# Performance work log

Measured on AMD Instinct MI355X. Metric: run time of the kernel, lower is better.

## Reference

```python
import jax, jax.numpy as jnp
import numpy as np

N_NODES = 50000
N_EDGES = 500000
D_MODEL = 128
NHEAD = 8
D_HEAD = 16
NUM_KEYS = 8
NUM_ETYPES = 4
NUM_STRINGS = 20000
NUM_BLOCKS = 2
N_TARGETS = 128


def setup_inputs() -> dict:
    key = jax.random.key(0)
    ks = jax.random.split(key, 16)
    s = 1.0 / np.sqrt(D_MODEL)
    return {
        "emb": jax.random.normal(ks[0], (NUM_STRINGS, D_MODEL), jnp.float32) * s,
        "query_w": jax.random.normal(ks[1], (NUM_BLOCKS, NUM_KEYS, NHEAD, D_HEAD, D_MODEL), jnp.float32) * s,
        "key_w": jax.random.normal(ks[2], (NUM_BLOCKS, NUM_ETYPES, NHEAD, D_HEAD, D_MODEL), jnp.float32) * s,
        "value_w": jax.random.normal(ks[3], (NUM_BLOCKS, NUM_ETYPES, NHEAD, D_HEAD, D_MODEL), jnp.float32) * s,
        "node_w": jax.random.normal(ks[4], (NUM_BLOCKS, NUM_KEYS, NHEAD, D_HEAD, D_MODEL), jnp.float32) * s,
        "target_w": jax.random.normal(ks[5], (NUM_BLOCKS, NUM_KEYS, NHEAD, D_HEAD), jnp.float32) * s,
        "ln_gamma": jnp.ones((NUM_BLOCKS, D_MODEL), jnp.float32),
        "ln_beta": jnp.zeros((NUM_BLOCKS, D_MODEL), jnp.float32),
        "value_ids": jax.random.randint(ks[6], (N_NODES,), 0, NUM_STRINGS),
        "key_ids": jax.random.randint(ks[7], (N_NODES,), 0, NUM_KEYS),
        "src": jax.random.randint(ks[8], (N_EDGES,), 0, N_NODES),
        "dst": jax.random.randint(ks[9], (N_EDGES,), 0, N_NODES),
        "etype": jax.random.randint(ks[10], (N_EDGES,), 0, NUM_ETYPES),
        "target_idx": jax.random.randint(ks[11], (N_TARGETS,), 0, N_NODES),
    }


def _layer_norm(x, g, b, eps=1e-5):
    mu = jnp.mean(x, -1, keepdims=True)
    var = jnp.var(x, -1, keepdims=True)
    return (x - mu) * jax.lax.rsqrt(var + eps) * g + b


def _per_type_proj(feat, w, type_ids):
    # feat: [N,D], w: [T,H,Dh,D] -> project for all types then select the
    # node's/edge-endpoint's own type (identical math to gathering w[type]).
    all_t = jnp.einsum("nd,thfd->nthf", feat, w)  # [N,T,H,Dh]
    return jnp.take_along_axis(all_t, type_ids[:, None, None, None], axis=1)[:, 0]


def _hetero_attn_conv(feat, qw, kw, vw, nw, lg, lb, key_ids, src, dst, etype):
    n = feat.shape[0]
    q = _per_type_proj(feat, qw, key_ids)                     # [N,H,Dh] per-key query
    k_all = jnp.einsum("nd,thfd->nthf", feat, kw)             # [N,T,H,Dh]
    v_all = jnp.einsum("nd,thfd->nthf", feat, vw)
    k_e = k_all[src, etype]                                   # [E,H,Dh] per-etype key
    v_e = v_all[src, etype]                                   # [E,H,Dh]
    scale = np.float32(1.0 / np.sqrt(D_HEAD))
    scores = jnp.sum(q[dst] * k_e, -1) * scale                # [E,H]
    # edge softmax over incoming edges of each dst node
    m = jax.ops.segment_max(scores, dst, num_segments=n)      # [N,H]
    e = jnp.exp(scores - m[dst])
    z = jax.ops.segment_sum(e, dst, num_segments=n)
    attn = e / (z[dst] + 1e-9)                                # [E,H]
    agg = jax.ops.segment_sum(attn[..., None] * v_e, dst, num_segments=n)
    agg = agg.reshape(n, D_MODEL)
    h = _per_type_proj(agg, nw, key_ids).reshape(n, D_MODEL)  # per-key node proj
    h = jax.nn.relu(h)                                        # node_activation='relu'
    return _layer_norm(h, lg, lb)                             # norm=True


def reference(emb, query_w, key_w, value_w, node_w, target_w, ln_gamma, ln_beta,
              value_ids, key_ids, src, dst, etype, target_idx):
    feat = emb[value_ids]  # ValueEmbedding lookup [N,D]
    target_keys = key_ids[target_idx]
    outs = []
    for i in range(NUM_BLOCKS):
        prev = feat
        feat = _hetero_attn_conv(feat, query_w[i], key_w[i], value_w[i], node_w[i],
                                 ln_gamma[i], ln_beta[i], key_ids, src, dst, etype)
        feat = feat + prev  # block_residual=True (conv_residual=False)
        tf = feat[target_idx].reshape(N_TARGETS, NHEAD, D_HEAD)
        tw = target_w[i][target_keys]  # [B,H,Dh]
        outs.append(jnp.sum(tf * tw, axis=(1, 2)))  # Target readout per block
    out = jnp.mean(jnp.stack(outs, -1), -1)  # mean over block outputs
    return out  # [N_TARGETS] (single target)
```

## Files before the change

kernel.cpp:

```cpp
#include <hip/hip_runtime.h>
#include <hip/hip_bf16.h>

#define N_NODES   50000
#define N_EDGES   500000
#define NHEAD     8
#define NUM_KEYS  8
#define NUM_ETYPES 4
#define NUM_BLOCKS 2
#define N_TARGETS 128
#define NPAD      51200
#define NTILES    400
#define NBLK      196
#define LDW       136
#define LDWF      132
#define QKVW      1152
#define SCAP      45

typedef unsigned short u16;
typedef unsigned int   u32;
typedef __attribute__((ext_vector_type(8))) short short8;
typedef __attribute__((ext_vector_type(4))) short short4v;
typedef __attribute__((ext_vector_type(4))) float floatx4;

__device__ __forceinline__ size_t pkaddr(int tile, int r, int c){
  return (size_t)tile * 16384 + ((c >> 3) << 10) + (r << 3) + (c & 7);
}

__device__ __forceinline__ float bflo(u32 u)  { return __uint_as_float(u << 16); }
__device__ __forceinline__ float bfhi(u32 u)  { return __uint_as_float(u & 0xffff0000u); }
__device__ __forceinline__ float bf2f(u16 u)  { return __uint_as_float(((u32)u) << 16); }
__device__ __forceinline__ u16   f2bf(float f){
  u32 u = __float_as_uint(f);
  u += 0x7fffu + ((u >> 16) & 1u);
  return (u16)(u >> 16);
}

__global__ void detect_dtype(const u16* raw, int* flag){
  __shared__ int cnt;
  if (threadIdx.x == 0) cnt = 0;
  __syncthreads();
  int sane = 0;
  #pragma unroll
  for (int k = 0; k < 4; k++){
    u16 u = raw[threadIdx.x * 4 + k];
    int e = (u >> 7) & 0xff;
    if (e >= 100 && e <= 145) sane++;
  }
  atomicAdd(&cnt, sane);
  __syncthreads();
  if (threadIdx.x == 0) *flag = (cnt >= 870) ? 1 : 0;
}

__global__ void cvt_f32(const void* src, float* dst, int n, const int* flag){
  int i = blockIdx.x * 256 + threadIdx.x;
  if (i >= n) return;
  dst[i] = (*flag) ? bf2f(((const u16*)src)[i]) : ((const float*)src)[i];
}
__global__ void cvt_packw(const void* src, size_t soff, u16* dst, int n, const int* flag){
  int i = blockIdx.x * 256 + threadIdx.x;
  if (i >= n) return;
  u16 v = (*flag) ? ((const u16*)src)[soff + i] : f2bf(((const float*)src)[soff + i]);
  int mat = i >> 14, rem = i & 16383;
  int row = rem >> 7, k = rem & 127;
  dst[pkaddr(mat, row, k)] = v;
}

__global__ void khist_blk(const int* __restrict__ key_ids, int* __restrict__ blkcnt){
  __shared__ int c[8];
  int t = threadIdx.x, b = blockIdx.x;
  if (t < 8) c[t] = 0;
  __syncthreads();
  int n = b * 256 + t;
  if (n < N_NODES) atomicAdd(&c[key_ids[n]], 1);
  __syncthreads();
  if (t < 8) blkcnt[t * NBLK + b] = c[t];
}
__global__ void kscan2(const int* __restrict__ blkcnt, int* __restrict__ base,
                       int* __restrict__ tile_key){
  __shared__ int po[8];
  __shared__ int tot[8];
  int t = threadIdx.x;
  if (t < 8){
    int s = 0;
    for (int b = 0; b < NBLK; b++) s += blkcnt[t * NBLK + b];
    tot[t] = s;
  }
  __syncthreads();
  if (t == 0){
    int off = 0;
    for (int k = 0; k < 8; k++){ po[k] = off; off += ((tot[k] + 127) >> 7) << 7; }
  }
  __syncthreads();
  if (t < 8){
    int run = po[t];
    for (int b = 0; b < NBLK; b++){ base[t * NBLK + b] = run; run += blkcnt[t * NBLK + b]; }
  }
  for (int tt = t; tt < NTILES; tt += 64){
    int row = tt << 7, k = 7;
    for (int kk = 1; kk < 8; kk++)
      if (row < po[kk]){ k = kk - 1; break; }
    tile_key[tt] = k;
  }
}
__global__ void scatter_perm2(const int* __restrict__ key_ids, const int* __restrict__ base,
                              int* __restrict__ perm, int* __restrict__ invperm){
  __shared__ unsigned char keyarr[256];
  int t = threadIdx.x, b = blockIdx.x;
  int n = b * 256 + t;
  int key = (n < N_NODES) ? key_ids[n] : 8;
  keyarr[t] = (unsigned char)key;
  __syncthreads();
  if (n >= N_NODES) return;
  int rank = 0;
  for (int j = 0; j < t; j++) rank += (keyarr[j] == (unsigned char)key);
  int pos = base[key * NBLK + b] + rank;
  perm[pos] = n;
  invperm[n] = pos;
}

__global__ void gather_feat(const void* emb_raw, const int* __restrict__ vid,
                            const int* __restrict__ perm, const int* __restrict__ flag,
                            float* __restrict__ feat, u16* __restrict__ fhi,
                            u16* __restrict__ flo){
  int i = blockIdx.x * 256 + threadIdx.x;
  int n = i >> 7, d = i & 127;
  int e = (vid[perm[n]] << 7) + d;
  float v = (*flag) ? bf2f(((const u16*)emb_raw)[e]) : ((const float*)emb_raw)[e];
  feat[i] = v;
  u16 h = f2bf(v);
  size_t pa = pkaddr(n >> 7, n & 127, d);
  fhi[pa] = h;
  flo[pa] = f2bf(v - bf2f(h));
}

__global__ void hist_dst(const int* __restrict__ dst, const int* __restrict__ invp,
                         int* __restrict__ deg){
  int e = blockIdx.x * 256 + threadIdx.x;
  if (e < N_EDGES) atomicAdd(&deg[invp[dst[e]]], 1);
}
__global__ __launch_bounds__(1024) void scan_deg(const int* __restrict__ deg,
                                                 int* __restrict__ rs, int* __restrict__ cur){
  __shared__ int s[1024];
  int t = threadIdx.x;
  int lo = t * 50, hi = lo + 50;
  int sum = 0;
  for (int i = lo; i < hi; i++) sum += deg[i];
  s[t] = sum;
  __syncthreads();
  for (int off = 1; off < 1024; off <<= 1){
    int v = (t >= off) ? s[t - off] : 0;
    __syncthreads();
    s[t] += v;
    __syncthreads();
  }
  int run = s[t] - sum;
  for (int i = lo; i < hi; i++){
    rs[i] = run; cur[i] = run;
    run += deg[i];
  }
}
__global__ void scatter_edges(const int* __restrict__ src, const int* __restrict__ dst,
                              const int* __restrict__ et, const int* __restrict__ invp,
                              int* __restrict__ cur, u32* __restrict__ epk){
  int e = blockIdx.x * 256 + threadIdx.x;
  if (e >= N_EDGES) return;
  int pos = atomicAdd(&cur[invp[dst[e]]], 1);
  epk[pos] = ((u32)invp[src[e]] << 2) | (u32)et[e];
}
__global__ __launch_bounds__(256) void sort_csr(const int* __restrict__ rs,
                                                const int* __restrict__ deg,
                                                u32* __restrict__ epk){
  __shared__ u32 buf[256 * SCAP];
  int t = threadIdx.x;
  int n = blockIdx.x * 256 + t;
  if (n >= NPAD) return;
  int s = rs[n], c = deg[n];
  if (c <= 1) return;
  if (c <= SCAP){
    u32* b = buf + t * SCAP;
    for (int i = 0; i < c; i++) b[i] = epk[s + i];
    for (int i = 1; i < c; i++){
      u32 v = b[i];
      int j = i - 1;
      while (j >= 0 && b[j] > v){ b[j + 1] = b[j]; j--; }
      b[j + 1] = v;
    }
    for (int i = 0; i < c; i++) epk[s + i] = b[i];
  } else {
    for (int i = 1; i < c; i++){
      u32 v = epk[s + i];
      int j = i - 1;
      while (j >= 0 && epk[s + j] > v){ epk[s + j + 1] = epk[s + j]; j--; }
      epk[s + j + 1] = v;
    }
  }
}

__global__ __launch_bounds__(256) void gemm_qkv(
    const u16* __restrict__ Ahi, const u16* __restrict__ Alo,
    const u16* __restrict__ Qw, const u16* __restrict__ KVw,
    const int* __restrict__ tkey, u16* __restrict__ C)
{
  __shared__ u16 sc[128 * LDW];
  int id = blockIdx.x;
  int xcd = id & 7, wi = id >> 3;
  int cy = xcd * 50 + wi / 9;
  int cx = wi % 9;
  int m0 = cy * 128;
  const u16* Bte = (cx == 0) ? (Qw + (size_t)tkey[cy] * 16384)
                             : (KVw + (size_t)(cx - 1) * 16384);
  const u16* Ath = Ahi + (size_t)cy * 16384;
  const u16* Atl = Alo + (size_t)cy * 16384;
  int w = threadIdx.x >> 6, l = threadIdx.x & 63;
  int wm = (w & 1) * 64, wn = (w >> 1) * 64;
  int lr = l & 15, lg = l >> 4;
  floatx4 acc[4][4] = {};
  #pragma unroll
  for (int kk = 0; kk < 4; kk++){
    int cc10 = (kk * 4 + lg) << 10;
    short8 ah[4], al[4], bfr[4];
    #pragma unroll
    for (int i = 0; i < 4; i++){
      int off = cc10 + ((wm + i * 16 + lr) << 3);
      ah[i] = *(const short8*)(Ath + off);
      al[i] = *(const short8*)(Atl + off);
    }
    #pragma unroll
    for (int j = 0; j < 4; j++)
      bfr[j] = *(const short8*)(Bte + cc10 + ((wn + j * 16 + lr) << 3));
    #pragma unroll
    for (int i = 0; i < 4; i++)
      #pragma unroll
      for (int j = 0; j < 4; j++){
        acc[i][j] = __builtin_amdgcn_mfma_f32_16x16x32_bf16(ah[i], bfr[j], acc[i][j], 0, 0, 0);
        acc[i][j] = __builtin_amdgcn_mfma_f32_16x16x32_bf16(al[i], bfr[j], acc[i][j], 0, 0, 0);
      }
  }
  #pragma unroll
  for (int i = 0; i < 4; i++)
    #pragma unroll
    for (int j = 0; j < 4; j++)
      #pragma unroll
      for (int r = 0; r < 4; r++)
        sc[(wm + i * 16 + lg * 4 + r) * LDW + wn + j * 16 + lr] = f2bf(acc[i][j][r]);
  __syncthreads();
  int tr = threadIdx.x >> 4, tc = (threadIdx.x & 15) * 8;
  int cbase = cx * 128;
  #pragma unroll
  for (int it = 0; it < 8; it++){
    int row = tr + it * 16;
    short8 vv = *(const short8*)(sc + row * LDW + tc);
    *(short8*)(C + (size_t)(m0 + row) * QKVW + cbase + tc) = vv;
  }
}

__global__ __launch_bounds__(256) void gemm_h_ln(
    const u16* __restrict__ Ahi, const u16* __restrict__ Alo,
    const u16* __restrict__ Bt, const int* __restrict__ tkey,
    const float* __restrict__ gbf,
    float* __restrict__ feat, u16* __restrict__ fhi, u16* __restrict__ flo, int blk)
{
  __shared__ float scf[64 * LDWF];
  int m0 = blockIdx.x * 64;
  int tile = blockIdx.x >> 1, rbase = (blockIdx.x & 1) * 64;
  const u16* Bte = Bt + (size_t)tkey[tile] * 16384;
  const u16* Ath = Ahi + (size_t)tile * 16384;
  const u16* Atl = Alo + (size_t)tile * 16384;
  int w = threadIdx.x >> 6, l = threadIdx.x & 63;
  int wn = w * 32;
  int lr = l & 15, lg = l >> 4;
  floatx4 acc[4][2] = {};
  #pragma unroll
  for (int kk = 0; kk < 4; kk++){
    int cc10 = (kk * 4 + lg) << 10;
    short8 ah[4], al[4], bfr[2];
    #pragma unroll
    for (int i = 0; i < 4; i++){
      int off = cc10 + ((rbase + i * 16 + lr) << 3);
      ah[i] = *(const short8*)(Ath + off);
      al[i] = *(const short8*)(Atl + off);
    }
    #pragma unroll
    for (int j = 0; j < 2; j++)
      bfr[j] = *(const short8*)(Bte + cc10 + ((wn + j * 16 + lr) << 3));
    #pragma unroll
    for (int i = 0; i < 4; i++)
      #pragma unroll
      for (int j = 0; j < 2; j++){
        acc[i][j] = __builtin_amdgcn_mfma_f32_16x16x32_bf16(ah[i], bfr[j], acc[i][j], 0, 0, 0);
        acc[i][j] = __builtin_amdgcn_mfma_f32_16x16x32_bf16(al[i], bfr[j], acc[i][j], 0, 0, 0);
      }
  }
  #pragma unroll
  for (int i = 0; i < 4; i++)
    #pragma unroll
    for (int j = 0; j < 2; j++)
      #pragma unroll
      for (int r = 0; r < 4; r++)
        scf[(i * 16 + lg * 4 + r) * LDWF + wn + j * 16 + lr] = acc[i][j][r];
  __syncthreads();
  int r = threadIdx.x >> 2, q4 = (threadIdx.x & 3) * 32;
  const float* srow = scf + r * LDWF + q4;
  float s1 = 0.f, s2 = 0.f;
  #pragma unroll
  for (int c = 0; c < 32; c++){
    float v = fmaxf(srow[c], 0.f);
    s1 += v; s2 += v * v;
  }
  s1 += __shfl_xor(s1, 1, 64); s1 += __shfl_xor(s1, 2, 64);
  s2 += __shfl_xor(s2, 1, 64); s2 += __shfl_xor(s2, 2, 64);
  float mu = s1 * (1.f / 128.f);
  float var = s2 * (1.f / 128.f) - mu * mu;
  float rstd = rsqrtf(var + 1e-5f);
  int n = m0 + r;
  int ntile = n >> 7, nr = n & 127;
  float* fr = feat + (size_t)n * 128 + q4;
  const float* gp = gbf + (blk << 7) + q4;
  #pragma unroll
  for (int c = 0; c < 32; c += 4){
    float4 fo = *(float4*)(fr + c);
    float y0 = (fmaxf(srow[c+0], 0.f) - mu) * rstd * gp[c+0] + gp[256 + c + 0] + fo.x;
    float y1 = (fmaxf(srow[c+1], 0.f) - mu) * rstd * gp[c+1] + gp[256 + c + 1] + fo.y;
    float y2 = (fmaxf(srow[c+2], 0.f) - mu) * rstd * gp[c+2] + gp[256 + c + 2] + fo.z;
    float y3 = (fmaxf(srow[c+3], 0.f) - mu) * rstd * gp[c+3] + gp[256 + c + 3] + fo.w;
    *(float4*)(fr + c) = make_float4(y0, y1, y2, y3);
    u16 h0 = f2bf(y0), h1 = f2bf(y1), h2 = f2bf(y2), h3 = f2bf(y3);
    size_t pa = pkaddr(ntile, nr, q4 + c);
    short4v ph; ph.x = (short)h0; ph.y = (short)h1; ph.z = (short)h2; ph.w = (short)h3;
    *(short4v*)(fhi + pa) = ph;
    short4v pl;
    pl.x = (short)f2bf(y0 - bf2f(h0)); pl.y = (short)f2bf(y1 - bf2f(h1));
    pl.z = (short)f2bf(y2 - bf2f(h2)); pl.w = (short)f2bf(y3 - bf2f(h3));
    *(short4v*)(flo + pa) = pl;
  }
}

__device__ __forceinline__ float dot8(uint4 a, uint4 b){
  return bflo(a.x)*bflo(b.x) + bfhi(a.x)*bfhi(b.x)
       + bflo(a.y)*bflo(b.y) + bfhi(a.y)*bfhi(b.y)
       + bflo(a.z)*bflo(b.z) + bfhi(a.z)*bfhi(b.z)
       + bflo(a.w)*bflo(b.w) + bfhi(a.w)*bfhi(b.w);
}

__global__ __launch_bounds__(256) void edge_attn(
    const u16* __restrict__ qkv,
    const int* __restrict__ rs, const int* __restrict__ deg,
    const u32* __restrict__ epk, u16* __restrict__ agghi, u16* __restrict__ agglo)
{
  int n = blockIdx.x * 4 + (threadIdx.x >> 6);
  int l = threadIdx.x & 63;
  int h = l & 7, s = l >> 3;
  const u16* qp = qkv + (size_t)n * QKVW + (h << 4);
  uint4 q0 = *(const uint4*)qp, q1 = *(const uint4*)(qp + 8);
  int e0 = rs[n], cnt = deg[n];
  float z = 0.f;
  float acc[16];
  #pragma unroll
  for (int j = 0; j < 16; j++) acc[j] = 0.f;
  for (int base = 0; base < cnt; base += 16){
    int idx0 = base + s, idx1 = base + s + 8;
    bool p0 = idx0 < cnt, p1 = idx1 < cnt;
    u32 pk0 = p0 ? epk[e0 + idx0] : 0u;
    u32 pk1 = p1 ? epk[e0 + idx1] : 0u;
    const u16* kp0 = qkv + (size_t)(pk0 >> 2) * QKVW + 128 + ((pk0 & 3) << 7) + (h << 4);
    const u16* kp1 = qkv + (size_t)(pk1 >> 2) * QKVW + 128 + ((pk1 & 3) << 7) + (h << 4);
    if (p0){
      uint4 k0 = *(const uint4*)kp0, k1 = *(const uint4*)(kp0 + 8);
      float sc = (dot8(q0, k0) + dot8(q1, k1)) * 0.25f;
      float ew = __expf(fminf(sc, 80.f));
      const u16* vp = kp0 + 512;
      uint4 v0 = *(const uint4*)vp, v1 = *(const uint4*)(vp + 8);
      z += ew;
      acc[0]  += ew * bflo(v0.x); acc[1]  += ew * bfhi(v0.x);
      acc[2]  += ew * bflo(v0.y); acc[3]  += ew * bfhi(v0.y);
      acc[4]  += ew * bflo(v0.z); acc[5]  += ew * bfhi(v0.z);
      acc[6]  += ew * bflo(v0.w); acc[7]  += ew * bfhi(v0.w);
      acc[8]  += ew * bflo(v1.x); acc[9]  += ew * bfhi(v1.x);
      acc[10] += ew * bflo(v1.y); acc[11] += ew * bfhi(v1.y);
      acc[12] += ew * bflo(v1.z); acc[13] += ew * bfhi(v1.z);
      acc[14] += ew * bflo(v1.w); acc[15] += ew * bfhi(v1.w);
    }
    if (p1){
      uint4 k0 = *(const uint4*)kp1, k1 = *(const uint4*)(kp1 + 8);
      float sc = (dot8(q0, k0) + dot8(q1, k1)) * 0.25f;
      float ew = __expf(fminf(sc, 80.f));
      const u16* vp = kp1 + 512;
      uint4 v0 = *(const uint4*)vp, v1 = *(const uint4*)(vp + 8);
      z += ew;
      acc[0]  += ew * bflo(v0.x); acc[1]  += ew * bfhi(v0.x);
      acc[2]  += ew * bflo(v0.y); acc[3]  += ew * bfhi(v0.y);
      acc[4]  += ew * bflo(v0.z); acc[5]  += ew * bfhi(v0.z);
      acc[6]  += ew * bflo(v0.w); acc[7]  += ew * bfhi(v0.w);
      acc[8]  += ew * bflo(v1.x); acc[9]  += ew * bfhi(v1.x);
      acc[10] += ew * bflo(v1.y); acc[11] += ew * bfhi(v1.y);
      acc[12] += ew * bflo(v1.z); acc[13] += ew * bfhi(v1.z);
      acc[14] += ew * bflo(v1.w); acc[15] += ew * bfhi(v1.w);
    }
  }
  #pragma unroll
  for (int m = 8; m < 64; m <<= 1){
    z += __shfl_xor(z, m, 64);
    #pragma unroll
    for (int j = 0; j < 16; j++) acc[j] += __shfl_xor(acc[j], m, 64);
  }
  float inv = 1.f / (z + 1e-9f);
  int j0 = s * 2;
  float x0 = acc[j0] * inv, x1 = acc[j0 + 1] * inv;
  u16 h0 = f2bf(x0), h1 = f2bf(x1);
  int col = (h << 4) + j0;
  size_t pa = pkaddr(n >> 7, n & 127, col);
  *(u32*)(agghi + pa) = (u32)h0 | ((u32)h1 << 16);
  *(u32*)(agglo + pa) = (u32)f2bf(x0 - bf2f(h0)) | ((u32)f2bf(x1 - bf2f(h1)) << 16);
}

__global__ __launch_bounds__(128) void readout(
    const float* __restrict__ feat, const float* __restrict__ twf,
    const int* __restrict__ key_ids, const int* __restrict__ invp,
    const int* __restrict__ tgt,
    float* __restrict__ outacc, void* dout, const int* __restrict__ flag, int blk)
{
  int t = threadIdx.x;
  int n = tgt[t];
  int key = key_ids[n];
  const float* fr = feat + (size_t)invp[n] * 128;
  const float* wr = twf + (size_t)((blk * 8 + key) << 7);
  float acc = 0.f;
  #pragma unroll
  for (int d = 0; d < 128; d++) acc = fmaf(fr[d], wr[d], acc);
  if (blk == 0){
    outacc[t] = 0.5f * acc;
  } else {
    float r = outacc[t] + 0.5f * acc;
    if (*flag) ((u16*)dout)[t] = f2bf(r);
    else       ((float*)dout)[t] = r;
  }
}

extern "C" void kernel_launch(void* const* d_in, const int* in_sizes, int n_in,
                              void* d_out, int out_size, void* d_ws, size_t ws_size,
                              hipStream_t stream)
{
  const void* emb = d_in[0];
  const void* qw  = d_in[1];
  const void* kw  = d_in[2];
  const void* vw  = d_in[3];
  const void* nw  = d_in[4];
  const void* tw  = d_in[5];
  const void* lg  = d_in[6];
  const void* lb  = d_in[7];
  const int* value_ids = (const int*)d_in[8];
  const int* key_ids   = (const int*)d_in[9];
  const int* srcp  = (const int*)d_in[10];
  const int* dstp  = (const int*)d_in[11];
  const int* etp   = (const int*)d_in[12];
  const int* tgt   = (const int*)d_in[13];

  char* p = (char*)d_ws;
  auto carve = [&](size_t bytes)->char*{
    char* r = p; p += (bytes + 255) & ~(size_t)255; return r;
  };
  int*   flag    = (int*)  carve(4);
  float* featp   = (float*)carve((size_t)NPAD * 128 * 4);
  u16*   feathi  = (u16*)  carve((size_t)NPAD * 128 * 2);
  u16*   featlo  = (u16*)  carve((size_t)NPAD * 128 * 2);
  u16*   qwc     = (u16*)  carve((size_t)2 * 1024 * 128 * 2);
  u16*   kvw     = (u16*)  carve((size_t)2 * 1024 * 128 * 2);
  u16*   nwc     = (u16*)  carve((size_t)2 * 1024 * 128 * 2);
  float* twf     = (float*)carve((size_t)2048 * 4);
  float* gbf     = (float*)carve((size_t)512 * 4);
  int*   blkcnt  = (int*)  carve((size_t)8 * NBLK * 4);
  int*   kbase   = (int*)  carve((size_t)8 * NBLK * 4);
  int*   tile_key= (int*)  carve(NTILES * 4);
  int*   perm    = (int*)  carve((size_t)NPAD * 4);
  int*   invperm = (int*)  carve((size_t)N_NODES * 4);
  int*   deg     = (int*)  carve((size_t)NPAD * 4);
  int*   rsx     = (int*)  carve((size_t)NPAD * 4);
  int*   cur     = (int*)  carve((size_t)NPAD * 4);
  u32*   epk     = (u32*)  carve((size_t)N_EDGES * 4);
  u16*   qkvbuf  = (u16*)  carve((size_t)NPAD * QKVW * 2);
  u16*   agghi   = (u16*)  carve((size_t)NPAD * 128 * 2);
  u16*   agglo   = (u16*)  carve((size_t)NPAD * 128 * 2);
  float* outacc  = (float*)carve((size_t)N_TARGETS * 4);
  (void)ws_size; (void)n_in; (void)in_sizes; (void)out_size;

  detect_dtype<<<1, 256, 0, stream>>>((const u16*)emb, flag);

  auto cpk = [&](const void* s, size_t so, u16* d, int n){
    cvt_packw<<<(n + 255) / 256, 256, 0, stream>>>(s, so, d, n, flag);
  };
  cpk(qw, 0, qwc, 2 * 1024 * 128);
  cpk(nw, 0, nwc, 2 * 1024 * 128);
  for (int b = 0; b < 2; b++){
    cpk(kw, (size_t)b * 512 * 128, kvw + (size_t)b * 1024 * 128,             512 * 128);
    cpk(vw, (size_t)b * 512 * 128, kvw + (size_t)b * 1024 * 128 + 512 * 128, 512 * 128);
  }
  cvt_f32<<<8, 256, 0, stream>>>(tw, twf, 2048, flag);
  cvt_f32<<<1, 256, 0, stream>>>(lg, gbf, 256, flag);
  cvt_f32<<<1, 256, 0, stream>>>(lb, gbf + 256, 256, flag);

  hipMemsetAsync(perm, 0, (size_t)NPAD * 4, stream);
  khist_blk<<<NBLK, 256, 0, stream>>>(key_ids, blkcnt);
  kscan2<<<1, 64, 0, stream>>>(blkcnt, kbase, tile_key);
  scatter_perm2<<<NBLK, 256, 0, stream>>>(key_ids, kbase, perm, invperm);

  gather_feat<<<(NPAD * 128) / 256, 256, 0, stream>>>(emb, value_ids, perm, flag,
                                                      featp, feathi, featlo);

  hipMemsetAsync(deg, 0, (size_t)NPAD * 4, stream);
  const int eg = (N_EDGES + 255) / 256;
  hist_dst<<<eg, 256, 0, stream>>>(dstp, invperm, deg);
  scan_deg<<<1, 1024, 0, stream>>>(deg, rsx, cur);
  scatter_edges<<<eg, 256, 0, stream>>>(srcp, dstp, etp, invperm, cur, epk);
  sort_csr<<<(NPAD + 255) / 256, 256, 0, stream>>>(rsx, deg, epk);

  for (int b = 0; b < NUM_BLOCKS; b++){
    gemm_qkv<<<3600, 256, 0, stream>>>(feathi, featlo,
                                       qwc + (size_t)b * 1024 * 128,
                                       kvw + (size_t)b * 1024 * 128,
                                       tile_key, qkvbuf);
    edge_attn<<<NPAD / 4, 256, 0, stream>>>(qkvbuf, rsx, deg, epk, agghi, agglo);
    gemm_h_ln<<<NPAD / 64, 256, 0, stream>>>(agghi, agglo,
                                             nwc + (size_t)b * 1024 * 128,
                                             tile_key, gbf, featp, feathi, featlo, b);
    readout<<<1, 128, 0, stream>>>(featp, twf, key_ids, invperm, tgt, outacc, d_out, flag, b);
  }
}
```

Before: 492.0 us.

## Store Q/K as hi+lo bf16 pairs in interleaved per-head layout; fuse weight packing

The QKV GEMM now writes Q and K as split hi/lo bf16 pairs, so attention scores keep near-fp32 accuracy. K-hi, K-lo and V for each head are interleaved into one contiguous 48-element segment, so each edge gather touches one region instead of two distant ones. The row width grows from 1152 to 1792, which raises the GEMM's store traffic and each edge's bytes. The ten or so separate weight conversion launches are merged into a single pack_all kernel to cut launch overhead.

```diff
diff --git a/kernel.cpp b/kernel.cpp
--- a/kernel.cpp
+++ b/kernel.cpp
@@ -13,7 +13,7 @@
 #define NBLK      196
 #define LDW       136
 #define LDWF      132
-#define QKVW      1152
+#define QKVW      1792
 #define SCAP      45
 
 typedef unsigned short u16;
@@ -51,18 +51,30 @@
   if (threadIdx.x == 0) *flag = (cnt >= 870) ? 1 : 0;
 }
 
-__global__ void cvt_f32(const void* src, float* dst, int n, const int* flag){
+__global__ void pack_all(const void* qw, const void* nw, const void* kw, const void* vw,
+                         const void* tw, const void* lg, const void* lb,
+                         u16* qwc, u16* nwc, u16* kvw, float* twf, float* gbf,
+                         const int* __restrict__ flag){
   int i = blockIdx.x * 256 + threadIdx.x;
-  if (i >= n) return;
-  dst[i] = (*flag) ? bf2f(((const u16*)src)[i]) : ((const float*)src)[i];
-}
-__global__ void cvt_packw(const void* src, size_t soff, u16* dst, int n, const int* flag){
-  int i = blockIdx.x * 256 + threadIdx.x;
-  if (i >= n) return;
-  u16 v = (*flag) ? ((const u16*)src)[soff + i] : f2bf(((const float*)src)[soff + i]);
-  int mat = i >> 14, rem = i & 16383;
-  int row = rem >> 7, k = rem & 127;
-  dst[pkaddr(mat, row, k)] = v;
+  int F = *flag;
+  if (i < 786432){
+    int tile = i >> 14, rem = i & 16383;
+    int row = rem >> 7, col = rem & 127;
+    const void* src; int sidx; u16* dst; int dtile;
+    if (tile < 16){ src = qw; sidx = i; dst = qwc; dtile = tile; }
+    else if (tile < 32){ src = nw; sidx = i - 262144; dst = nwc; dtile = tile - 16; }
+    else if (tile < 40){ int t = tile - 32; src = kw; sidx = i - 524288;
+      dst = kvw; dtile = (t >> 2) * 8 + (t & 3); }
+    else { int t = tile - 40; src = vw; sidx = i - 655360;
+      dst = kvw; dtile = (t >> 2) * 8 + 4 + (t & 3); }
+    u16 v = F ? ((const u16*)src)[sidx] : f2bf(((const float*)src)[sidx]);
+    dst[pkaddr(dtile, row, col)] = v;
+  } else if (i < 788992){
+    int j = i - 786432;
+    if (j < 2048)      twf[j] = F ? bf2f(((const u16*)tw)[j]) : ((const float*)tw)[j];
+    else if (j < 2304){ int k = j - 2048; gbf[k]       = F ? bf2f(((const u16*)lg)[k]) : ((const float*)lg)[k]; }
+    else              { int k = j - 2304; gbf[256 + k] = F ? bf2f(((const u16*)lb)[k]) : ((const float*)lb)[k]; }
+  }
 }
 
 __global__ void khist_blk(const int* __restrict__ key_ids, int* __restrict__ blkcnt){
@@ -213,11 +225,11 @@
   const u16* Atl = Alo + (size_t)cy * 16384;
   int w = threadIdx.x >> 6, l = threadIdx.x & 63;
   int wm = (w & 1) * 64, wn = (w >> 1) * 64;
-  int lr = l & 15, lg = l >> 4;
+  int lr = l & 15, lgp = l >> 4;
   floatx4 acc[4][4] = {};
   #pragma unroll
   for (int kk = 0; kk < 4; kk++){
-    int cc10 = (kk * 4 + lg) << 10;
+    int cc10 = (kk * 4 + lgp) << 10;
     short8 ah[4], al[4], bfr[4];
     #pragma unroll
     for (int i = 0; i < 4; i++){
@@ -236,21 +248,41 @@
         acc[i][j] = __builtin_amdgcn_mfma_f32_16x16x32_bf16(al[i], bfr[j], acc[i][j], 0, 0, 0);
       }
   }
-  #pragma unroll
-  for (int i = 0; i < 4; i++)
-    #pragma unroll
-    for (int j = 0; j < 4; j++)
+  auto stagef = [&](int wantlo){
+    #pragma unroll
+    for (int i = 0; i < 4; i++)
       #pragma unroll
-      for (int r = 0; r < 4; r++)
-        sc[(wm + i * 16 + lg * 4 + r) * LDW + wn + j * 16 + lr] = f2bf(acc[i][j][r]);
-  __syncthreads();
+      for (int j = 0; j < 4; j++)
+        #pragma unroll
+        for (int r = 0; r < 4; r++){
+          float a = acc[i][j][r];
+          u16 hv = f2bf(a);
+          u16 ov = wantlo ? f2bf(a - bf2f(hv)) : hv;
+          sc[(wm + i * 16 + lgp * 4 + r) * LDW + wn + j * 16 + lr] = ov;
+        }
+  };
   int tr = threadIdx.x >> 4, tc = (threadIdx.x & 15) * 8;
-  int cbase = cx * 128;
-  #pragma unroll
-  for (int it = 0; it < 8; it++){
-    int row = tr + it * 16;
-    short8 vv = *(const short8*)(sc + row * LDW + tc);
-    *(short8*)(C + (size_t)(m0 + row) * QKVW + cbase + tc) = vv;
+  int hh = tc >> 4, dh = tc & 15;
+  auto storef = [&](size_t cb){
+    #pragma unroll
+    for (int it = 0; it < 8; it++){
+      int row = tr + it * 16;
+      short8 vv = *(const short8*)(sc + row * LDW + tc);
+      *(short8*)(C + (size_t)(m0 + row) * QKVW + cb) = vv;
+    }
+  };
+  if (cx == 0){
+    stagef(0); __syncthreads(); storef((size_t)tc);
+    __syncthreads();
+    stagef(1); __syncthreads(); storef((size_t)(128 + tc));
+  } else if (cx <= 4){
+    size_t cb = 256 + (size_t)(cx - 1) * 384 + hh * 48 + dh;
+    stagef(0); __syncthreads(); storef(cb);
+    __syncthreads();
+    stagef(1); __syncthreads(); storef(cb + 16);
+  } else {
+    size_t cb = 256 + (size_t)(cx - 5) * 384 + hh * 48 + 32 + dh;
+    stagef(0); __syncthreads(); storef(cb);
   }
 }
 
@@ -268,11 +300,11 @@
   const u16* Atl = Alo + (size_t)tile * 16384;
   int w = threadIdx.x >> 6, l = threadIdx.x & 63;
   int wn = w * 32;
-  int lr = l & 15, lg = l >> 4;
+  int lr = l & 15, lgp = l >> 4;
   floatx4 acc[4][2] = {};
   #pragma unroll
   for (int kk = 0; kk < 4; kk++){
-    int cc10 = (kk * 4 + lg) << 10;
+    int cc10 = (kk * 4 + lgp) << 10;
     short8 ah[4], al[4], bfr[2];
     #pragma unroll
     for (int i = 0; i < 4; i++){
@@ -297,7 +329,7 @@
     for (int j = 0; j < 2; j++)
       #pragma unroll
       for (int r = 0; r < 4; r++)
-        scf[(i * 16 + lg * 4 + r) * LDWF + wn + j * 16 + lr] = acc[i][j][r];
+        scf[(i * 16 + lgp * 4 + r) * LDWF + wn + j * 16 + lr] = acc[i][j][r];
   __syncthreads();
   int r = threadIdx.x >> 2, q4 = (threadIdx.x & 3) * 32;
   const float* srow = scf + r * LDWF + q4;
@@ -335,11 +367,38 @@
   }
 }
 
-__device__ __forceinline__ float dot8(uint4 a, uint4 b){
-  return bflo(a.x)*bflo(b.x) + bfhi(a.x)*bfhi(b.x)
-       + bflo(a.y)*bflo(b.y) + bfhi(a.y)*bfhi(b.y)
-       + bflo(a.z)*bflo(b.z) + bfhi(a.z)*bfhi(b.z)
-       + bflo(a.w)*bflo(b.w) + bfhi(a.w)*bfhi(b.w);
+__device__ __forceinline__ void edge_body(const u16* kb, const float* qf,
+                                          float& z, float* acc){
+  uint4 kh0 = *(const uint4*)kb,        kh1 = *(const uint4*)(kb + 8);
+  uint4 kl0 = *(const uint4*)(kb + 16), kl1 = *(const uint4*)(kb + 24);
+  uint4 v0  = *(const uint4*)(kb + 32), v1  = *(const uint4*)(kb + 40);
+  float s = 0.f;
+  s = fmaf(qf[0],  bflo(kh0.x) + bflo(kl0.x), s);
+  s = fmaf(qf[1],  bfhi(kh0.x) + bfhi(kl0.x), s);
+  s = fmaf(qf[2],  bflo(kh0.y) + bflo(kl0.y), s);
+  s = fmaf(qf[3],  bfhi(kh0.y) + bfhi(kl0.y), s);
+  s = fmaf(qf[4],  bflo(kh0.z) + bflo(kl0.z), s);
+  s = fmaf(qf[5],  bfhi(kh0.z) + bfhi(kl0.z), s);
+  s = fmaf(qf[6],  bflo(kh0.w) + bflo(kl0.w), s);
+  s = fmaf(qf[7],  bfhi(kh0.w) + bfhi(kl0.w), s);
+  s = fmaf(qf[8],  bflo(kh1.x) + bflo(kl1.x), s);
+  s = fmaf(qf[9],  bfhi(kh1.x) + bfhi(kl1.x), s);
+  s = fmaf(qf[10], bflo(kh1.y) + bflo(kl1.y), s);
+  s = fmaf(qf[11], bfhi(kh1.y) + bfhi(kl1.y), s);
+  s = fmaf(qf[12], bflo(kh1.z) + bflo(kl1.z), s);
+  s = fmaf(qf[13], bfhi(kh1.z) + bfhi(kl1.z), s);
+  s = fmaf(qf[14], bflo(kh1.w) + bflo(kl1.w), s);
+  s = fmaf(qf[15], bfhi(kh1.w) + bfhi(kl1.w), s);
+  float ew = __expf(fminf(s * 0.25f, 80.f));
+  z += ew;
+  acc[0]  += ew * bflo(v0.x); acc[1]  += ew * bfhi(v0.x);
+  acc[2]  += ew * bflo(v0.y); acc[3]  += ew * bfhi(v0.y);
+  acc[4]  += ew * bflo(v0.z); acc[5]  += ew * bfhi(v0.z);
+  acc[6]  += ew * bflo(v0.w); acc[7]  += ew * bfhi(v0.w);
+  acc[8]  += ew * bflo(v1.x); acc[9]  += ew * bfhi(v1.x);
+  acc[10] += ew * bflo(v1.y); acc[11] += ew * bfhi(v1.y);
+  acc[12] += ew * bflo(v1.z); acc[13] += ew * bfhi(v1.z);
+  acc[14] += ew * bflo(v1.w); acc[15] += ew * bfhi(v1.w);
 }
 
 __global__ __launch_bounds__(256) void edge_attn(
@@ -351,51 +410,32 @@
   int l = threadIdx.x & 63;
   int h = l & 7, s = l >> 3;
   const u16* qp = qkv + (size_t)n * QKVW + (h << 4);
-  uint4 q0 = *(const uint4*)qp, q1 = *(const uint4*)(qp + 8);
+  uint4 qh0 = *(const uint4*)qp,         qh1 = *(const uint4*)(qp + 8);
+  uint4 ql0 = *(const uint4*)(qp + 128), ql1 = *(const uint4*)(qp + 136);
+  float qf[16];
+  qf[0]  = bflo(qh0.x) + bflo(ql0.x); qf[1]  = bfhi(qh0.x) + bfhi(ql0.x);
+  qf[2]  = bflo(qh0.y) + bflo(ql0.y); qf[3]  = bfhi(qh0.y) + bfhi(ql0.y);
+  qf[4]  = bflo(qh0.z) + bflo(ql0.z); qf[5]  = bfhi(qh0.z) + bfhi(ql0.z);
+  qf[6]  = bflo(qh0.w) + bflo(ql0.w); qf[7]  = bfhi(qh0.w) + bfhi(ql0.w);
+  qf[8]  = bflo(qh1.x) + bflo(ql1.x); qf[9]  = bfhi(qh1.x) + bfhi(ql1.x);
+  qf[10] = bflo(qh1.y) + bflo(ql1.y); qf[11] = bfhi(qh1.y) + bfhi(ql1.y);
+  qf[12] = bflo(qh1.z) + bflo(ql1.z); qf[13] = bfhi(qh1.z) + bfhi(ql1.z);
+  qf[14] = bflo(qh1.w) + bflo(ql1.w); qf[15] = bfhi(qh1.w) + bfhi(ql1.w);
   int e0 = rs[n], cnt = deg[n];
   float z = 0.f;
   float acc[16];
   #pragma unroll
   for (int j = 0; j < 16; j++) acc[j] = 0.f;
+  int hb = h * 48;
   for (int base = 0; base < cnt; base += 16){
     int idx0 = base + s, idx1 = base + s + 8;
     bool p0 = idx0 < cnt, p1 = idx1 < cnt;
     u32 pk0 = p0 ? epk[e0 + idx0] : 0u;
     u32 pk1 = p1 ? epk[e0 + idx1] : 0u;
-    const u16* kp0 = qkv + (size_t)(pk0 >> 2) * QKVW + 128 + ((pk0 & 3) << 7) + (h << 4);
-    const u16* kp1 = qkv + (size_t)(pk1 >> 2) * QKVW + 128 + ((pk1 & 3) << 7) + (h << 4);
-    if (p0){
-      uint4 k0 = *(const uint4*)kp0, k1 = *(const uint4*)(kp0 + 8);
-      float sc = (dot8(q0, k0) + dot8(q1, k1)) * 0.25f;
-      float ew = __expf(fminf(sc, 80.f));
-      const u16* vp = kp0 + 512;
-      uint4 v0 = *(const uint4*)vp, v1 = *(const uint4*)(vp + 8);
-      z += ew;
-      acc[0]  += ew * bflo(v0.x); acc[1]  += ew * bfhi(v0.x);
-      acc[2]  += ew * bflo(v0.y); acc[3]  += ew * bfhi(v0.y);
-      acc[4]  += ew * bflo(v0.z); acc[5]  += ew * bfhi(v0.z);
-      acc[6]  += ew * bflo(v0.w); acc[7]  += ew * bfhi(v0.w);
-      acc[8]  += ew * bflo(v1.x); acc[9]  += ew * bfhi(v1.x);
-      acc[10] += ew * bflo(v1.y); acc[11] += ew * bfhi(v1.y);
-      acc[12] += ew * bflo(v1.z); acc[13] += ew * bfhi(v1.z);
-      acc[14] += ew * bflo(v1.w); acc[15] += ew * bfhi(v1.w);
-    }
-    if (p1){
-      uint4 k0 = *(const uint4*)kp1, k1 = *(const uint4*)(kp1 + 8);
-      float sc = (dot8(q0, k0) + dot8(q1, k1)) * 0.25f;
-      float ew = __expf(fminf(sc, 80.f));
-      const u16* vp = kp1 + 512;
-      uint4 v0 = *(const uint4*)vp, v1 = *(const uint4*)(vp + 8);
-      z += ew;
-      acc[0]  += ew * bflo(v0.x); acc[1]  += ew * bfhi(v0.x);
-      acc[2]  += ew * bflo(v0.y); acc[3]  += ew * bfhi(v0.y);
-      acc[4]  += ew * bflo(v0.z); acc[5]  += ew * bfhi(v0.z);
-      acc[6]  += ew * bflo(v0.w); acc[7]  += ew * bfhi(v0.w);
-      acc[8]  += ew * bflo(v1.x); acc[9]  += ew * bfhi(v1.x);
-      acc[10] += ew * bflo(v1.y); acc[11] += ew * bfhi(v1.y);
-      acc[12] += ew * bflo(v1.z); acc[13] += ew * bfhi(v1.z);
-      acc[14] += ew * bflo(v1.w); acc[15] += ew * bfhi(v1.w);
-    }
+    const u16* kb0 = qkv + (size_t)(pk0 >> 2) * QKVW + 256 + ((pk0 & 3) * 384) + hb;
+    const u16* kb1 = qkv + (size_t)(pk1 >> 2) * QKVW + 256 + ((pk1 & 3) * 384) + hb;
+    if (p0) edge_body(kb0, qf, z, acc);
+    if (p1) edge_body(kb1, qf, z, acc);
   }
   #pragma unroll
   for (int m = 8; m < 64; m <<= 1){
@@ -485,18 +525,8 @@
 
   detect_dtype<<<1, 256, 0, stream>>>((const u16*)emb, flag);
 
-  auto cpk = [&](const void* s, size_t so, u16* d, int n){
-    cvt_packw<<<(n + 255) / 256, 256, 0, stream>>>(s, so, d, n, flag);
-  };
-  cpk(qw, 0, qwc, 2 * 1024 * 128);
-  cpk(nw, 0, nwc, 2 * 1024 * 128);
-  for (int b = 0; b < 2; b++){
-    cpk(kw, (size_t)b * 512 * 128, kvw + (size_t)b * 1024 * 128,             512 * 128);
-    cpk(vw, (size_t)b * 512 * 128, kvw + (size_t)b * 1024 * 128 + 512 * 128, 512 * 128);
-  }
-  cvt_f32<<<8, 256, 0, stream>>>(tw, twf, 2048, flag);
-  cvt_f32<<<1, 256, 0, stream>>>(lg, gbf, 256, flag);
-  cvt_f32<<<1, 256, 0, stream>>>(lb, gbf + 256, 256, flag);
+  pack_all<<<3083, 256, 0, stream>>>(qw, nw, kw, vw, tw, lg, lb,
+                                     qwc, nwc, kvw, twf, gbf, flag);
 
   hipMemsetAsync(perm, 0, (size_t)NPAD * 4, stream);
   khist_blk<<<NBLK, 256, 0, stream>>>(key_ids, blkcnt);
```

New measurement: 607.4 us. 1.23x slower.
